# Performance work log

Hardware: AMD Instinct MI355X
Metric: run time of the kernel (lower is better)

Reference implementation:

```python
import jax, jax.numpy as jnp
import numpy as np
from jax import lax

VOCAB, EMB, HID, OUT = 50000, 300, 1024, 20
BATCH, SEQ = 256, 128


def setup_inputs() -> dict:
    key = jax.random.key(0)
    ks = jax.random.split(key, 10)
    cat = HID + EMB  # concat order is (c_prev, xt)
    s_gate = 1.0 / np.sqrt(cat)
    s_pred = 1.0 / np.sqrt(HID)
    return {
        "x": jax.random.randint(ks[0], (BATCH, SEQ), 0, VOCAB, dtype=jnp.int32),
        "emb": jax.random.normal(ks[1], (VOCAB, EMB), dtype=jnp.float32),
        "W_r": jax.random.uniform(ks[2], (HID, cat), minval=-s_gate, maxval=s_gate, dtype=jnp.float32),
        "b_r": jax.random.uniform(ks[3], (HID,), minval=-s_gate, maxval=s_gate, dtype=jnp.float32),
        "W_u": jax.random.uniform(ks[4], (HID, cat), minval=-s_gate, maxval=s_gate, dtype=jnp.float32),
        "b_u": jax.random.uniform(ks[5], (HID,), minval=-s_gate, maxval=s_gate, dtype=jnp.float32),
        "W_c": jax.random.uniform(ks[6], (HID, cat), minval=-s_gate, maxval=s_gate, dtype=jnp.float32),
        "b_c": jax.random.uniform(ks[7], (HID,), minval=-s_gate, maxval=s_gate, dtype=jnp.float32),
        "W_p": jax.random.uniform(ks[8], (OUT, HID), minval=-s_pred, maxval=s_pred, dtype=jnp.float32),
        "b_p": jax.random.uniform(ks[9], (OUT,), minval=-s_pred, maxval=s_pred, dtype=jnp.float32),
    }


def reference(x, emb, W_r, b_r, W_u, b_u, W_c, b_c, W_p, b_p):
    # x: [B, T] int ids -> embed to [B, T, E]
    xe = emb[x]
    B = x.shape[0]
    H = W_r.shape[0]

    def step(c_prev, xt):
        # concat order matches torch.cat((c_prev, xt), 1)
        cg = jnp.concatenate([c_prev, xt], axis=-1)           # [B, H+E]
        rt = jax.nn.sigmoid(cg @ W_r.T + b_r)                 # [B, H]
        ut = jax.nn.sigmoid(cg @ W_u.T + b_u)                 # [B, H]
        cc = jnp.concatenate([rt * c_prev, xt], axis=-1)      # [B, H+E]
        cct = jnp.tanh(cc @ W_c.T + b_c)                      # [B, H]
        c_next = ut * cct + (1.0 - ut) * c_prev               # [B, H]
        yt = c_next @ W_p.T + b_p                             # [B, OUT]
        return c_next, yt

    c0 = jnp.zeros((B, H), dtype=xe.dtype)
    _, y = lax.scan(step, c0, jnp.swapaxes(xe, 0, 1))         # y: [T, B, OUT]
    return jnp.swapaxes(y, 0, 1)                              # [B, T, OUT]
```

## Files before the change

### kernel.cpp

```cpp
#include <hip/hip_runtime.h>
#include <stdint.h>

typedef _Float16 f16;
typedef _Float16 f16x8 __attribute__((ext_vector_type(8)));
typedef float f32x4 __attribute__((ext_vector_type(4)));

#define BATCH 256
#define SEQ   128
#define EMB   300
#define HID   1024
#define OUTD  20
#define CAT   1324
#define KE    1344
#define XP    320
#define LSTR  1352
#define LSX   328
#define BPG   32
#define MPG   32

__device__ __forceinline__ float sigm(float z)  { return 1.f / (1.f + __expf(-z)); }
__device__ __forceinline__ float tanhf_(float z){ float e = __expf(2.f * z); return 1.f - 2.f / (e + 1.f); }

#define MFMA(a,b,c) __builtin_amdgcn_mfma_f32_16x16x32_f16((a),(b),(c),0,0,0)

#define ALOAD64(p) __hip_atomic_load((const unsigned long long*)(p), \
                                     __ATOMIC_RELAXED, __HIP_MEMORY_SCOPE_AGENT)

__device__ __forceinline__ void gld8_sc0(f16x8 (&A)[8], const f16* p)
{
    asm volatile(
        "global_load_dwordx4 %0, %8, off sc0\n\t"
        "global_load_dwordx4 %1, %8, off offset:64 sc0\n\t"
        "global_load_dwordx4 %2, %8, off offset:128 sc0\n\t"
        "global_load_dwordx4 %3, %8, off offset:192 sc0\n\t"
        "global_load_dwordx4 %4, %8, off offset:256 sc0\n\t"
        "global_load_dwordx4 %5, %8, off offset:320 sc0\n\t"
        "global_load_dwordx4 %6, %8, off offset:384 sc0\n\t"
        "global_load_dwordx4 %7, %8, off offset:448 sc0\n\t"
        "s_waitcnt vmcnt(0)"
        : "=&v"(A[0]), "=&v"(A[1]), "=&v"(A[2]), "=&v"(A[3]),
          "=&v"(A[4]), "=&v"(A[5]), "=&v"(A[6]), "=&v"(A[7])
        : "v"(p)
        : "memory");
}
__device__ __forceinline__ void gld4_f32_sc0(float (&r)[4], const float* p0, const float* p1,
                                             const float* p2, const float* p3)
{
    asm volatile(
        "global_load_dword %0, %4, off sc0\n\t"
        "global_load_dword %1, %5, off sc0\n\t"
        "global_load_dword %2, %6, off sc0\n\t"
        "global_load_dword %3, %7, off sc0\n\t"
        "s_waitcnt vmcnt(0)"
        : "=&v"(r[0]), "=&v"(r[1]), "=&v"(r[2]), "=&v"(r[3])
        : "v"(p0), "v"(p1), "v"(p2), "v"(p3)
        : "memory");
}
__device__ __forceinline__ void gst_f16_sc0(f16* p, f16 v)
{
    union { f16 h; unsigned short u; } cv; cv.h = v;
    unsigned int w = cv.u;
    asm volatile("global_store_short %0, %1, off sc0" :: "v"(p), "v"(w) : "memory");
}
__device__ __forceinline__ void gst_f32_sc0(float* p, float v)
{
    asm volatile("global_store_dword %0, %1, off sc0" :: "v"(p), "v"(v) : "memory");
}

__global__ void pack_kernel(const float* __restrict__ Wr, const float* __restrict__ br,
                            const float* __restrict__ Wu, const float* __restrict__ bu,
                            const float* __restrict__ Wc, const float* __restrict__ bc,
                            const float* __restrict__ Wp,
                            f16* __restrict__ Wru_e, f16* __restrict__ Wc_e, f16* __restrict__ Wp_e)
{
    const int NRU = 2048 * KE, NC = 1024 * KE, NP = 32 * HID;
    for (int idx = blockIdx.x * blockDim.x + threadIdx.x; idx < NRU + NC + NP;
         idx += gridDim.x * blockDim.x) {
        if (idx < NRU) {
            int n = idx / KE, k = idx - n * KE;
            const float* Ws = (n < HID) ? Wr : Wu;
            const float* bs = (n < HID) ? br : bu;
            int row = n & (HID - 1);
            float v = (k < CAT) ? Ws[(size_t)row * CAT + k] : ((k == CAT) ? bs[row] : 0.f);
            Wru_e[idx] = (f16)v;
        } else if (idx < NRU + NC) {
            int j = idx - NRU;
            int n = j / KE, k = j - n * KE;
            float v = (k < CAT) ? Wc[(size_t)n * CAT + k] : ((k == CAT) ? bc[n] : 0.f);
            Wc_e[j] = (f16)v;
        } else {
            int j = idx - NRU - NC;
            int n = j / HID, k = j & (HID - 1);
            Wp_e[j] = (n < OUTD) ? (f16)Wp[(size_t)n * HID + k] : (f16)(0.f);
        }
    }
}

__global__ void gather_kernel(const int* __restrict__ x, const float* __restrict__ emb,
                              f16* __restrict__ xe)
{
    const int TOT = SEQ * BATCH * XP;
    for (int idx = blockIdx.x * blockDim.x + threadIdx.x; idx < TOT;
         idx += gridDim.x * blockDim.x) {
        int e  = idx % XP;
        int rb = idx / XP;
        int b  = rb & 255, t = rb >> 8;
        float v;
        if (e < EMB) { int id = x[b * SEQ + t]; v = emb[(size_t)id * EMB + e]; }
        else          v = (e == EMB) ? 1.f : 0.f;
        xe[idx] = (f16)v;
    }
}

__global__ void zero_kernel(uint32_t* __restrict__ c0, int n0, uint32_t* __restrict__ bar, int nb)
{
    for (int i = blockIdx.x * blockDim.x + threadIdx.x; i < n0; i += gridDim.x * blockDim.x)
        c0[i] = 0u;
    if (blockIdx.x == 0)
        for (int i = threadIdx.x; i < nb; i += blockDim.x) bar[i] = 0u;
}

__device__ __forceinline__ void bar_arrive(int* slot, int ep, int fast)
{
    __syncthreads();
    if (threadIdx.x == 0) {
        if (fast) {
            *(volatile int*)slot = ep;
        } else {
            __builtin_amdgcn_fence(__ATOMIC_RELEASE, "agent");
            __hip_atomic_store(slot, ep, __ATOMIC_RELAXED, __HIP_MEMORY_SCOPE_AGENT);
        }
    }
}
__device__ __forceinline__ void bar_check(int* arrg, int* go, int ep, int fast, int lane)
{
    int spins = 0;
    if (fast) {
        while (!__all(*(volatile int*)&arrg[lane & 31] >= ep)) {
            __builtin_amdgcn_s_sleep(1);
            if (++spins > (1 << 24)) break;
        }
        __builtin_amdgcn_fence(__ATOMIC_ACQ_REL, "workgroup");
        if (lane == 0) *(volatile int*)go = ep;
    } else {
        while (!__all(__hip_atomic_load(&arrg[lane & 31], __ATOMIC_RELAXED,
                                        __HIP_MEMORY_SCOPE_AGENT) >= ep)) {
            __builtin_amdgcn_s_sleep(1);
            if (++spins > (1 << 24)) break;
        }
        __builtin_amdgcn_fence(__ATOMIC_ACQUIRE, "agent");
        __builtin_amdgcn_fence(__ATOMIC_RELEASE, "agent");
        if (lane == 0)
            __hip_atomic_store(go, ep, __ATOMIC_RELAXED, __HIP_MEMORY_SCOPE_AGENT);
    }
}
__device__ __forceinline__ void bar_wait(int* go, int ep, int fast)
{
    if (threadIdx.x == 0) {
        int spins = 0;
        if (fast) {
            while (*(volatile int*)go < ep) {
                __builtin_amdgcn_s_sleep(1);
                if (++spins > (1 << 24)) break;
            }
            __builtin_amdgcn_fence(__ATOMIC_ACQUIRE, "workgroup");
        } else {
            while (__hip_atomic_load(go, __ATOMIC_RELAXED, __HIP_MEMORY_SCOPE_AGENT) < ep) {
                __builtin_amdgcn_s_sleep(1);
                if (++spins > (1 << 24)) break;
            }
            __builtin_amdgcn_fence(__ATOMIC_ACQUIRE, "agent");
        }
    }
    __syncthreads();
}

__device__ __forceinline__ void kloop2(const f16* __restrict__ a0, const f16* __restrict__ a1,
                                       const f16* bp, f32x4& acc0, f32x4& acc1)
{
    f16x8 A0[2][8], A1[2][8], B[2][8];
    #pragma unroll
    for (int i = 0; i < 8; ++i) {
        A0[0][i] = *(const f16x8*)(a0 + i * 32);
        A1[0][i] = *(const f16x8*)(a1 + i * 32);
        B [0][i] = *(const f16x8*)(bp + i * 32);
    }
    #pragma unroll
    for (int h = 0; h < 4; ++h) {
        const int cur = h & 1, nxt = cur ^ 1;
        if (h < 3) {
            #pragma unroll
            for (int i = 0; i < 8; ++i) {
                const int kc = (h + 1) * 8 + i;
                A0[nxt][i] = *(const f16x8*)(a0 + kc * 32);
                A1[nxt][i] = *(const f16x8*)(a1 + kc * 32);
                B [nxt][i] = *(const f16x8*)(bp + kc * 32);
            }
        }
        #pragma unroll
        for (int i = 0; i < 8; ++i) {
            acc0 = MFMA(A0[cur][i], B[cur][i], acc0);
            acc1 = MFMA(A1[cur][i], B[cur][i], acc1);
        }
    }
}
__device__ __forceinline__ void kloop1s(const f16* a, const f16* bp, f32x4& acc)
{
    #pragma unroll
    for (int h = 0; h < 4; ++h) {
        f16x8 B[8], A[8];
        #pragma unroll
        for (int i = 0; i < 8; ++i) B[i] = *(const f16x8*)(bp + (h * 8 + i) * 32);
        gld8_sc0(A, a + h * 256);
        #pragma unroll
        for (int i = 0; i < 8; ++i) acc = MFMA(A[i], B[i], acc);
    }
}
__device__ __forceinline__ void kloop1a(const f16* a, const f16* bp, f32x4& acc)
{
    union Frag { unsigned long long u[2]; f16x8 v; };
    #pragma unroll
    for (int h = 0; h < 4; ++h) {
        Frag A[8]; f16x8 B[8];
        #pragma unroll
        for (int i = 0; i < 8; ++i) {
            const f16* p = a + (h * 8 + i) * 32;
            A[i].u[0] = ALOAD64(p);
            A[i].u[1] = ALOAD64(p + 4);
            B[i] = *(const f16x8*)(bp + (h * 8 + i) * 32);
        }
        #pragma unroll
        for (int i = 0; i < 8; ++i) acc = MFMA(A[i].v, B[i], acc);
    }
}
__device__ __forceinline__ void xpart2(const f16* xa0, const f16* xa1, const f16* bx,
                                       f32x4& acc0, f32x4& acc1)
{
    #pragma unroll
    for (int kc = 0; kc < 10; ++kc) {
        f16x8 B = *(const f16x8*)(bx + kc * 32);
        acc0 = MFMA(*(const f16x8*)(xa0 + kc * 32), B, acc0);
        acc1 = MFMA(*(const f16x8*)(xa1 + kc * 32), B, acc1);
    }
}
__device__ __forceinline__ void xpart1(const f16* xa, const f16* bx, f32x4& acc)
{
    #pragma unroll
    for (int kc = 0; kc < 10; ++kc)
        acc = MFMA(*(const f16x8*)(xa + kc * 32),
                   *(const f16x8*)(bx + kc * 32), acc);
}

__global__ __launch_bounds__(256, 1) void rnn_kernel(
    const f16* __restrict__ xe,  const f16* __restrict__ Wru,
    const f16* __restrict__ Wc,  const f16* __restrict__ Wp,
    const float* __restrict__ bpred, f16* __restrict__ Call,
    float* __restrict__ U, f16* __restrict__ RC,
    int* __restrict__ bar, float* __restrict__ out)
{
    extern __shared__ char smem[];
    f16* ldsRU = (f16*)smem;
    f16* ldsC  = ldsRU + 32 * LSTR;
    f16* ldsX  = ldsC  + 16 * LSTR;
    __shared__ int s_g, s_r, s_fast;

    const int tid  = threadIdx.x;
    const int lane = tid & 63;
    const int wv   = tid >> 6;
    const int q    = lane >> 4;
    const int cx   = lane & 15;
    const int ko   = q * 8;

    if (tid == 0) {
        int xcd = (int)__builtin_amdgcn_s_getreg((31 << 11) | 20) & 15;
        int r   = __hip_atomic_fetch_add(&bar[xcd], 1, __ATOMIC_RELAXED,
                                         __HIP_MEMORY_SCOPE_AGENT);
        __builtin_amdgcn_fence(__ATOMIC_RELEASE, "agent");
        __hip_atomic_fetch_add(&bar[16], 1, __ATOMIC_RELAXED, __HIP_MEMORY_SCOPE_AGENT);
        int spins = 0;
        while (__hip_atomic_load(&bar[16], __ATOMIC_RELAXED, __HIP_MEMORY_SCOPE_AGENT) < 256) {
            __builtin_amdgcn_s_sleep(1);
            if (++spins > (1 << 24)) break;
        }
        __builtin_amdgcn_fence(__ATOMIC_ACQUIRE, "agent");
        int ok = 1;
        for (int i = 0; i < 8; ++i) ok &= (bar[i] == BPG);
        if (ok) { s_g = xcd; s_r = r; s_fast = 1; }
        else    { s_g = blockIdx.x & 7; s_r = blockIdx.x >> 3; s_fast = 0; }
    }
    __syncthreads();
    const int g    = s_g;
    const int gblk = s_r;
    const int fast = s_fast;
    const int mG   = g * MPG;
    const int N0   = gblk * 64;
    const int M0   = gblk * 32;
    const int jm   = wv & 1;

    int* arrg = bar + 64 + g * BPG;
    int* slot = arrg + gblk;
    int* go   = bar + 384 + g * 16;

    {
        const f16* gRU = Wru + (size_t)N0 * KE;
        for (int i = tid; i < 32 * (KE / 8); i += 256) {
            int r = i / (KE / 8), c = i % (KE / 8);
            *(f16x8*)(ldsRU + r * LSTR + c * 8) = *(const f16x8*)(gRU + (size_t)r * KE + c * 8);
        }
        const f16* gC = Wc + (size_t)M0 * KE;
        for (int i = tid; i < 16 * (KE / 8); i += 256) {
            int r = i / (KE / 8), c = i % (KE / 8);
            *(f16x8*)(ldsC + r * LSTR + c * 8) = *(const f16x8*)(gC + (size_t)r * KE + c * 8);
        }
        for (int i = tid; i < 48 * (XP / 8); i += 256) {
            int r = i / (XP / 8), c = i % (XP / 8);
            const f16* src = (r < 32)
                ? (Wru + (size_t)(N0 + 32 + r) * KE + 1024 + c * 8)
                : (Wc  + (size_t)(M0 + 16 + (r - 32)) * KE + 1024 + c * 8);
            *(f16x8*)(ldsX + r * LSX + c * 8) = *(const f16x8*)src;
        }
        __syncthreads();
    }

    const f16* bG = (wv < 2) ? (const f16*)(ldsRU + (size_t)(wv * 16 + cx) * LSTR + ko)
                             : (const f16*)(Wru + (size_t)(N0 + wv * 16 + cx) * KE + ko);
    const f16* bU = (wv < 2) ? (const f16*)(ldsC + (size_t)cx * LSTR + ko)
                             : (const f16*)(Wc + (size_t)(M0 + 16 + cx) * KE + ko);
    const f16* bGx = (wv < 2) ? bG + 1024
                              : (const f16*)(ldsX + (size_t)((wv - 2) * 16 + cx) * LSX + ko);
    const f16* bUx = (wv < 2) ? bU + 1024
                              : (const f16*)(ldsX + (size_t)(32 + cx) * LSX + ko);
    const int nG = N0 + wv * 16 + cx;
    const int nU = M0 + (wv >> 1) * 16 + cx;
    const int is_chk = (gblk == 0 && wv == 0);

    f32x4 gx0 = {0.f,0.f,0.f,0.f}, gx1 = {0.f,0.f,0.f,0.f};
    xpart2(xe + (size_t)(mG + cx) * XP + ko,
           xe + (size_t)(mG + 16 + cx) * XP + ko, bGx, gx0, gx1);

    int ep = 0;
    for (int t = 0; t < SEQ; ++t) {
        const f16* Ct  = Call + (size_t)t * BATCH * HID;
        f16*       Ct1 = Call + (size_t)(t + 1) * BATCH * HID;
        const f16* xet = xe   + (size_t)t * BATCH * XP;

        {
            float cpf[2][4];
            if (N0 < HID) {
                #pragma unroll
                for (int jt = 0; jt < 2; ++jt)
                    #pragma unroll
                    for (int r = 0; r < 4; ++r)
                        cpf[jt][r] = (float)Ct[(size_t)(mG + jt * 16 + q * 4 + r) * HID + nG];
            }
            f32x4 acc0 = gx0, acc1 = gx1;
            kloop2(Ct + (size_t)(mG + cx) * HID + ko,
                   Ct + (size_t)(mG + 16 + cx) * HID + ko, bG, acc0, acc1);
            if (N0 < HID) {
                #pragma unroll
                for (int jt = 0; jt < 2; ++jt) {
                    const f32x4& ac = jt ? acc1 : acc0;
                    #pragma unroll
                    for (int r = 0; r < 4; ++r) {
                        int m = mG + jt * 16 + q * 4 + r;
                        f16 vv = (f16)(sigm(ac[r]) * cpf[jt][r]);
                        if (fast) gst_f16_sc0(&RC[(size_t)m * HID + nG], vv);
                        else      *(volatile f16*)&RC[(size_t)m * HID + nG] = vv;
                    }
                }
            } else {
                #pragma unroll
                for (int jt = 0; jt < 2; ++jt) {
                    const f32x4& ac = jt ? acc1 : acc0;
                    #pragma unroll
                    for (int r = 0; r < 4; ++r) {
                        int m = mG + jt * 16 + q * 4 + r;
                        float uv = sigm(ac[r]);
                        if (fast) gst_f32_sc0(&U[(size_t)m * HID + (nG - HID)], uv);
                        else __hip_atomic_store(&U[(size_t)m * HID + (nG - HID)], uv,
                                                __ATOMIC_RELAXED, __HIP_MEMORY_SCOPE_AGENT);
                    }
                }
            }
        }
        ++ep;
        bar_arrive(slot, ep, fast);
        f32x4 ux = {0.f,0.f,0.f,0.f};
        if (is_chk) {
            bar_check(arrg, go, ep, fast, lane);
            xpart1(xet + (size_t)(mG + jm * 16 + cx) * XP + ko, bUx, ux);
        } else {
            xpart1(xet + (size_t)(mG + jm * 16 + cx) * XP + ko, bUx, ux);
        }
        bar_wait(go, ep, fast);

        {
            float uu[4], cold[4];
            {
                int m0 = mG + jm * 16 + q * 4;
                if (fast) {
                    gld4_f32_sc0(uu, &U[(size_t)m0 * HID + nU],
                                     &U[(size_t)(m0 + 1) * HID + nU],
                                     &U[(size_t)(m0 + 2) * HID + nU],
                                     &U[(size_t)(m0 + 3) * HID + nU]);
                } else {
                    #pragma unroll
                    for (int r = 0; r < 4; ++r)
                        uu[r] = __hip_atomic_load(&U[(size_t)(m0 + r) * HID + nU],
                                                  __ATOMIC_RELAXED, __HIP_MEMORY_SCOPE_AGENT);
                }
                #pragma unroll
                for (int r = 0; r < 4; ++r)
                    cold[r] = (float)Ct[(size_t)(m0 + r) * HID + nU];
            }
            f32x4 acc = ux;
            const f16* a = RC + (size_t)(mG + jm * 16 + cx) * HID + ko;
            if (fast) kloop1s(a, bU, acc);
            else      kloop1a(a, bU, acc);
            #pragma unroll
            for (int r = 0; r < 4; ++r) {
                int m = mG + jm * 16 + q * 4 + r;
                float cct = tanhf_(acc[r]);
                f16 cv = (f16)(uu[r] * cct + (1.f - uu[r]) * cold[r]);
                if (fast) gst_f16_sc0(&Ct1[(size_t)m * HID + nU], cv);
                else      *(volatile f16*)&Ct1[(size_t)m * HID + nU] = cv;
            }
        }
        ++ep;
        bar_arrive(slot, ep, fast);
        gx0 = (f32x4){0.f,0.f,0.f,0.f};
        gx1 = (f32x4){0.f,0.f,0.f,0.f};
        if (is_chk) {
            bar_check(arrg, go, ep, fast, lane);
            if (t + 1 < SEQ)
                xpart2(xe + (size_t)(t + 1) * BATCH * XP + (size_t)(mG + cx) * XP + ko,
                       xe + (size_t)(t + 1) * BATCH * XP + (size_t)(mG + 16 + cx) * XP + ko,
                       bGx, gx0, gx1);
        } else {
            if (t + 1 < SEQ)
                xpart2(xe + (size_t)(t + 1) * BATCH * XP + (size_t)(mG + cx) * XP + ko,
                       xe + (size_t)(t + 1) * BATCH * XP + (size_t)(mG + 16 + cx) * XP + ko,
                       bGx, gx0, gx1);
        }
        bar_wait(go, ep, fast);
    }

    #pragma unroll
    for (int i = 0; i < 2; ++i) {
        const int mt = gblk * 8 + wv * 2 + i;
        const int tt = mt >> 1;
        const int bb = mG + (mt & 1) * 16;
        const f16* ap  = Call + (size_t)(tt + 1) * BATCH * HID + (size_t)(bb + cx) * HID + ko;
        const f16* wp0 = Wp + (size_t)cx * HID + ko;
        const f16* wp1 = Wp + (size_t)(16 + cx) * HID + ko;
        f32x4 acc0 = {0.f,0.f,0.f,0.f}, acc1 = {0.f,0.f,0.f,0.f};
        f16x8 A[8], B0[8], B1[8];
        #pragma unroll
        for (int h = 0; h < 4; ++h) {
            #pragma unroll
            for (int j2 = 0; j2 < 8; ++j2) {
                const int kc = h * 8 + j2;
                A[j2]  = *(const f16x8*)(ap  + kc * 32);
                B0[j2] = *(const f16x8*)(wp0 + kc * 32);
                B1[j2] = *(const f16x8*)(wp1 + kc * 32);
            }
            #pragma unroll
            for (int j2 = 0; j2 < 8; ++j2) {
                acc0 = MFMA(A[j2], B0[j2], acc0);
                acc1 = MFMA(A[j2], B1[j2], acc1);
            }
        }
        #pragma unroll
        for (int nt = 0; nt < 2; ++nt) {
            const int o = nt * 16 + cx;
            if (o < OUTD) {
                const f32x4& ac = nt ? acc1 : acc0;
                #pragma unroll
                for (int r = 0; r < 4; ++r) {
                    const int brow = bb + q * 4 + r;
                    out[((size_t)brow * SEQ + tt) * OUTD + o] = ac[r] + bpred[o];
                }
            }
        }
    }
}

extern "C" void kernel_launch(void* const* d_in, const int* in_sizes, int n_in,
                              void* d_out, int out_size, void* d_ws, size_t ws_size,
                              hipStream_t stream)
{
    const int*   x   = (const int*)  d_in[0];
    const float* emb = (const float*)d_in[1];
    const float* Wr  = (const float*)d_in[2];
    const float* br  = (const float*)d_in[3];
    const float* Wu  = (const float*)d_in[4];
    const float* bu  = (const float*)d_in[5];
    const float* Wc  = (const float*)d_in[6];
    const float* bc  = (const float*)d_in[7];
    const float* Wp  = (const float*)d_in[8];
    const float* bp  = (const float*)d_in[9];

    char* p = (char*)d_ws;
    int* bar   = (int*)p;  p += 1024 * sizeof(int);
    f16* Wru_e = (f16*)p;  p += (size_t)2048 * KE * 2;
    f16* Wc_e  = (f16*)p;  p += (size_t)1024 * KE * 2;
    f16* Wp_e  = (f16*)p;  p += (size_t)32 * HID * 2;
    f16* xe    = (f16*)p;  p += (size_t)SEQ * BATCH * XP * 2;
    f16* Call  = (f16*)p;  p += (size_t)(SEQ + 1) * BATCH * HID * 2;
    float* U   = (float*)p; p += (size_t)BATCH * HID * 4;
    f16* RC    = (f16*)p;  p += (size_t)BATCH * HID * 2;

    const int LDS_BYTES = 48 * LSTR * 2 + 48 * LSX * 2;

    pack_kernel<<<2048, 256, 0, stream>>>(Wr, br, Wu, bu, Wc, bc, Wp, Wru_e, Wc_e, Wp_e);
    gather_kernel<<<4096, 256, 0, stream>>>(x, emb, xe);
    zero_kernel<<<256, 256, 0, stream>>>((uint32_t*)Call, BATCH * HID / 2, (uint32_t*)bar, 1024);

    hipFuncSetAttribute((const void*)rnn_kernel,
                        hipFuncAttributeMaxDynamicSharedMemorySize, LDS_BYTES);

    void* args[] = { &xe, &Wru_e, &Wc_e, &Wp_e, (void*)&bp, &Call, &U, &RC, &bar, &d_out };
    hipLaunchCooperativeKernel((const void*)rnn_kernel, dim3(256), dim3(256),
                               args, LDS_BYTES, stream);
}
```

Measured before the change: 2.999 ms.

## Replace two-level grid barrier with per-block polling of arrival slots

Removes the checker-block/go-flag two-stage barrier. Each block's wave 0 now polls all 32 arrival slots of its group directly, which cuts one round-trip through a shared go flag on every barrier. The x-projection work (xpart1/xpart2) moves to before the arrive instead of overlapping the wait. The trade-off is more polling traffic on the arrival slots, since 32 blocks each read 32 slots, and the x-work no longer hides the barrier latency.

```diff
diff --git a/kernel.cpp b/kernel.cpp
--- a/kernel.cpp
+++ b/kernel.cpp
@@ -132,40 +132,19 @@
         }
     }
 }
-__device__ __forceinline__ void bar_check(int* arrg, int* go, int ep, int fast, int lane)
-{
-    int spins = 0;
-    if (fast) {
-        while (!__all(*(volatile int*)&arrg[lane & 31] >= ep)) {
-            __builtin_amdgcn_s_sleep(1);
-            if (++spins > (1 << 24)) break;
-        }
-        __builtin_amdgcn_fence(__ATOMIC_ACQ_REL, "workgroup");
-        if (lane == 0) *(volatile int*)go = ep;
-    } else {
-        while (!__all(__hip_atomic_load(&arrg[lane & 31], __ATOMIC_RELAXED,
-                                        __HIP_MEMORY_SCOPE_AGENT) >= ep)) {
-            __builtin_amdgcn_s_sleep(1);
-            if (++spins > (1 << 24)) break;
-        }
-        __builtin_amdgcn_fence(__ATOMIC_ACQUIRE, "agent");
-        __builtin_amdgcn_fence(__ATOMIC_RELEASE, "agent");
-        if (lane == 0)
-            __hip_atomic_store(go, ep, __ATOMIC_RELAXED, __HIP_MEMORY_SCOPE_AGENT);
-    }
-}
-__device__ __forceinline__ void bar_wait(int* go, int ep, int fast)
-{
-    if (threadIdx.x == 0) {
+__device__ __forceinline__ void bar_poll(int* arrg, int ep, int fast, int wv, int lane)
+{
+    if (wv == 0) {
         int spins = 0;
         if (fast) {
-            while (*(volatile int*)go < ep) {
+            while (!__all(*(volatile int*)&arrg[lane & 31] >= ep)) {
                 __builtin_amdgcn_s_sleep(1);
                 if (++spins > (1 << 24)) break;
             }
             __builtin_amdgcn_fence(__ATOMIC_ACQUIRE, "workgroup");
         } else {
-            while (__hip_atomic_load(go, __ATOMIC_RELAXED, __HIP_MEMORY_SCOPE_AGENT) < ep) {
+            while (!__all(__hip_atomic_load(&arrg[lane & 31], __ATOMIC_RELAXED,
+                                            __HIP_MEMORY_SCOPE_AGENT) >= ep)) {
                 __builtin_amdgcn_s_sleep(1);
                 if (++spins > (1 << 24)) break;
             }
@@ -299,7 +278,6 @@
 
     int* arrg = bar + 64 + g * BPG;
     int* slot = arrg + gblk;
-    int* go   = bar + 384 + g * 16;
 
     {
         const f16* gRU = Wru + (size_t)N0 * KE;
@@ -332,7 +310,6 @@
                               : (const f16*)(ldsX + (size_t)(32 + cx) * LSX + ko);
     const int nG = N0 + wv * 16 + cx;
     const int nU = M0 + (wv >> 1) * 16 + cx;
-    const int is_chk = (gblk == 0 && wv == 0);
 
     f32x4 gx0 = {0.f,0.f,0.f,0.f}, gx1 = {0.f,0.f,0.f,0.f};
     xpart2(xe + (size_t)(mG + cx) * XP + ko,
@@ -383,16 +360,11 @@
                 }
             }
         }
+        f32x4 ux = {0.f,0.f,0.f,0.f};
+        xpart1(xet + (size_t)(mG + jm * 16 + cx) * XP + ko, bUx, ux);
         ++ep;
         bar_arrive(slot, ep, fast);
-        f32x4 ux = {0.f,0.f,0.f,0.f};
-        if (is_chk) {
-            bar_check(arrg, go, ep, fast, lane);
-            xpart1(xet + (size_t)(mG + jm * 16 + cx) * XP + ko, bUx, ux);
-        } else {
-            xpart1(xet + (size_t)(mG + jm * 16 + cx) * XP + ko, bUx, ux);
-        }
-        bar_wait(go, ep, fast);
+        bar_poll(arrg, ep, fast, wv, lane);
 
         {
             float uu[4], cold[4];
@@ -426,23 +398,15 @@
                 else      *(volatile f16*)&Ct1[(size_t)m * HID + nU] = cv;
             }
         }
+        gx0 = (f32x4){0.f,0.f,0.f,0.f};
+        gx1 = (f32x4){0.f,0.f,0.f,0.f};
+        if (t + 1 < SEQ)
+            xpart2(xe + (size_t)(t + 1) * BATCH * XP + (size_t)(mG + cx) * XP + ko,
+                   xe + (size_t)(t + 1) * BATCH * XP + (size_t)(mG + 16 + cx) * XP + ko,
+                   bGx, gx0, gx1);
         ++ep;
         bar_arrive(slot, ep, fast);
-        gx0 = (f32x4){0.f,0.f,0.f,0.f};
-        gx1 = (f32x4){0.f,0.f,0.f,0.f};
-        if (is_chk) {
-            bar_check(arrg, go, ep, fast, lane);
-            if (t + 1 < SEQ)
-                xpart2(xe + (size_t)(t + 1) * BATCH * XP + (size_t)(mG + cx) * XP + ko,
-                       xe + (size_t)(t + 1) * BATCH * XP + (size_t)(mG + 16 + cx) * XP + ko,
-                       bGx, gx0, gx1);
-        } else {
-            if (t + 1 < SEQ)
-                xpart2(xe + (size_t)(t + 1) * BATCH * XP + (size_t)(mG + cx) * XP + ko,
-                       xe + (size_t)(t + 1) * BATCH * XP + (size_t)(mG + 16 + cx) * XP + ko,
-                       bGx, gx0, gx1);
-        }
-        bar_wait(go, ep, fast);
+        bar_poll(arrg, ep, fast, wv, lane);
     }
 
     #pragma unroll
```

Result: slower. 3.157 ms (+5.3%).
